# Kernel tuning notes

Measured on AMD Instinct MI355X. Metric: run time of the kernel, lower is better.

Reference implementation:

```python
import jax, jax.numpy as jnp
import numpy as np

N, E, IN, HID, HEADS, ED, OUT = 50000, 600000, 128, 64, 4, 16, 2
NEG_SLOPE = 0.2  # PyG GATv2Conv default negative_slope


def glorot(key, shape):
    fan_in, fan_out = shape[0], shape[-1]
    s = jnp.sqrt(6.0 / (fan_in + fan_out))
    return jax.random.uniform(key, shape, jnp.float32, -s, s)


def setup_inputs() -> dict:
    key = jax.random.key(0)
    ks = jax.random.split(key, 16)
    return {
        "x": jax.random.normal(ks[0], (N, IN), jnp.float32),
        "edge_index": jax.random.randint(ks[1], (2, E), 0, N, jnp.int32),
        "edge_attr": jax.random.normal(ks[2], (E, ED), jnp.float32),
        # conv1: GATv2Conv(IN -> HID, heads=HEADS, concat=True, edge_dim=ED)
        "W1l": glorot(ks[3], (IN, HEADS * HID)), "b1l": jnp.zeros((HEADS * HID,), jnp.float32),
        "W1r": glorot(ks[4], (IN, HEADS * HID)), "b1r": jnp.zeros((HEADS * HID,), jnp.float32),
        "W1e": glorot(ks[5], (ED, HEADS * HID)), "b1e": jnp.zeros((HEADS * HID,), jnp.float32),
        "att1": glorot(ks[6], (HEADS, HID)),
        "bias1": jnp.zeros((HEADS * HID,), jnp.float32),
        # conv2: GATv2Conv(HEADS*HID -> HID, heads=1, concat=False, edge_dim=ED)
        "W2l": glorot(ks[7], (HEADS * HID, HID)), "b2l": jnp.zeros((HID,), jnp.float32),
        "W2r": glorot(ks[8], (HEADS * HID, HID)), "b2r": jnp.zeros((HID,), jnp.float32),
        "W2e": glorot(ks[9], (ED, HID)), "b2e": jnp.zeros((HID,), jnp.float32),
        "att2": glorot(ks[10], (1, HID)),
        "bias2": jnp.zeros((HID,), jnp.float32),
        # edge MLP: Linear(2*HID+ED -> HID) -> ReLU -> Linear(HID -> OUT)
        "Wm1": glorot(ks[11], (2 * HID + ED, HID)), "bm1": jnp.zeros((HID,), jnp.float32),
        "Wm2": glorot(ks[12], (HID, OUT)), "bm2": jnp.zeros((OUT,), jnp.float32),
    }


def gatv2_layer(x, src, dst, edge_attr, Wl, bl, Wr, br, We, be, att, bias, heads, ch, concat):
    n = x.shape[0]
    xl = (x @ Wl + bl).reshape(n, heads, ch)          # lin_l(source)
    xr = (x @ Wr + br).reshape(n, heads, ch)          # lin_r(target)
    xe = (edge_attr @ We + be).reshape(-1, heads, ch)  # lin_edge(edge_attr)
    m = jax.nn.leaky_relu(xl[src] + xr[dst] + xe, NEG_SLOPE)   # [E, H, C]
    logits = jnp.einsum('ehc,hc->eh', m, att)                  # [E, H]
    # segment softmax over incoming edges of each target node
    amax = jax.lax.stop_gradient(jax.ops.segment_max(logits, dst, num_segments=n))
    ex = jnp.exp(logits - amax[dst])
    denom = jax.ops.segment_sum(ex, dst, num_segments=n)
    alpha = ex / denom[dst]                                    # [E, H]
    out = jax.ops.segment_sum(xl[src] * alpha[..., None], dst, num_segments=n)  # [N, H, C]
    out = out.reshape(n, heads * ch) if concat else out.mean(axis=1)
    return out + bias


def reference(x, edge_index, edge_attr, W1l, b1l, W1r, b1r, W1e, b1e, att1, bias1,
              W2l, b2l, W2r, b2r, W2e, b2e, att2, bias2, Wm1, bm1, Wm2, bm2):
    src, dst = edge_index[0], edge_index[1]
    h = jax.nn.relu(gatv2_layer(x, src, dst, edge_attr, W1l, b1l, W1r, b1r, W1e, b1e, att1, bias1, HEADS, HID, True))
    h = jax.nn.relu(gatv2_layer(h, src, dst, edge_attr, W2l, b2l, W2r, b2r, W2e, b2e, att2, bias2, 1, HID, False))
    ef = jnp.concatenate([h[src], h[dst], edge_attr], axis=1)  # [E, 2*HID+ED]
    return jax.nn.relu(ef @ Wm1 + bm1) @ Wm2 + bm2             # [E, OUT]
```

## Files before the change

kernel.cpp:

```cpp
#include <hip/hip_runtime.h>
#include <math.h>

#define NN 50000
#define EE 600000
#define IND 128
#define HIDD 64
#define NH 4
#define EDD 16
#define OUTD 2
#define C1 256

typedef _Float16 h2 __attribute__((ext_vector_type(2)));

__device__ __forceinline__ unsigned short f2bf(float f){
    unsigned b = __float_as_uint(f);
    b += 0x7FFF + ((b >> 16) & 1);
    return (unsigned short)(b >> 16);
}
__device__ __forceinline__ float bf2f(unsigned short h){
    return __uint_as_float(((unsigned)h) << 16);
}
__device__ __forceinline__ h2 f2h2(float a, float b){
    h2 r; r[0] = (_Float16)a; r[1] = (_Float16)b; return r;
}

#if defined(__has_builtin)
#if __has_builtin(__builtin_amdgcn_fdot2)
#define HAS_FDOT2 1
#endif
#if __has_builtin(__builtin_amdgcn_exp2f)
#define HAS_EXP2 1
#endif
#endif
__device__ __forceinline__ float fdot2(h2 a, h2 b, float c){
#ifdef HAS_FDOT2
    return __builtin_amdgcn_fdot2(a, b, c, false);
#else
    return fmaf((float)a[1], (float)b[1], fmaf((float)a[0], (float)b[0], c));
#endif
}
__device__ __forceinline__ float fexp2(float x){
#ifdef HAS_EXP2
    return __builtin_amdgcn_exp2f(x);
#else
    return __expf(x * 0.69314718056f);
#endif
}

__global__ __launch_bounds__(256) void k_hist(const int* __restrict__ dst, int* __restrict__ cnt)
{
    int stride = gridDim.x * blockDim.x;
    for (int e = blockIdx.x * blockDim.x + threadIdx.x; e < EE; e += stride)
        atomicAdd(&cnt[dst[e]], 1);
}

__global__ __launch_bounds__(1024) void k_scan(const int* __restrict__ cnt, int* __restrict__ rs)
{
    __shared__ int wsum[16];
    __shared__ int wpref[16];
    int t = threadIdx.x, lane = t & 63, w = t >> 6;
    int running = 0;
    for (int base = 0; base < NN; base += 1024) {
        int idx = base + t;
        int v = (idx < NN) ? cnt[idx] : 0;
        int sc = v;
#pragma unroll
        for (int off = 1; off < 64; off <<= 1) {
            int u = __shfl_up(sc, off, 64);
            if (lane >= off) sc += u;
        }
        if (lane == 63) wsum[w] = sc;
        __syncthreads();
        if (w == 0 && lane < 16) {
            int x = wsum[lane];
#pragma unroll
            for (int off = 1; off < 16; off <<= 1) {
                int u = __shfl_up(x, off, 64);
                if (lane >= off) x += u;
            }
            wpref[lane] = x;
        }
        __syncthreads();
        int woff = (w == 0) ? 0 : wpref[w - 1];
        if (idx < NN) rs[idx] = running + woff + sc - v;
        running += wpref[15];
        __syncthreads();
    }
    if (t == 0) rs[NN] = running;
}

__global__ __launch_bounds__(256) void k_scatter(
    const int* __restrict__ src, const int* __restrict__ dst,
    const float* __restrict__ ea,
    const int* __restrict__ rs, int* __restrict__ cur,
    int* __restrict__ esrc, _Float16* __restrict__ ea_s, _Float16* __restrict__ ea_h)
{
    int stride = gridDim.x * blockDim.x;
    for (int e = blockIdx.x * blockDim.x + threadIdx.x; e < EE; e += stride) {
        int d = dst[e];
        int p = rs[d] + atomicAdd(&cur[d], 1);
        esrc[p] = src[e];
        const float4* s4 = (const float4*)(ea + (size_t)e * EDD);
        float4 a0 = s4[0], a1 = s4[1], a2 = s4[2], a3 = s4[3];
        union { h2 h[8]; uint4 u[2]; } pk;
        pk.h[0] = f2h2(a0.x, a0.y); pk.h[1] = f2h2(a0.z, a0.w);
        pk.h[2] = f2h2(a1.x, a1.y); pk.h[3] = f2h2(a1.z, a1.w);
        pk.h[4] = f2h2(a2.x, a2.y); pk.h[5] = f2h2(a2.z, a2.w);
        pk.h[6] = f2h2(a3.x, a3.y); pk.h[7] = f2h2(a3.z, a3.w);
        uint4* dq = (uint4*)(ea_s + (size_t)p * EDD);
        dq[0] = pk.u[0]; dq[1] = pk.u[1];
        uint4* hq = (uint4*)(ea_h + (size_t)e * EDD);
        hq[0] = pk.u[0]; hq[1] = pk.u[1];
    }
}

__global__ __launch_bounds__(256) void k_lin1(
    const float* __restrict__ x, const float* __restrict__ Wl, const float* __restrict__ bl,
    const float* __restrict__ Wr, const float* __restrict__ br,
    unsigned short* __restrict__ xl, float* __restrict__ xr)
{
    __shared__ h2 As[32 * 64];
    int t = threadIdx.x;
    int row0 = blockIdx.x * 32;
#pragma unroll
    for (int j = 0; j < 4; ++j) {
        int idx = t + j * 256;
        int r = idx >> 5, c4 = (idx & 31) * 4;
        float4 v = (row0 + r < NN) ? *((const float4*)(x + (size_t)(row0 + r) * IND + c4))
                                   : make_float4(0.f, 0.f, 0.f, 0.f);
        union { h2 h[2]; uint2 u; } pk;
        pk.h[0] = f2h2(v.x, v.y); pk.h[1] = f2h2(v.z, v.w);
        *((uint2*)&As[r * 64 + (c4 >> 1)]) = pk.u;
    }
    __syncthreads();
    float accl[32], accr[32];
    float bL = bl[t], bR = br[t];
#pragma unroll
    for (int i = 0; i < 32; ++i) { accl[i] = bL; accr[i] = bR; }
    for (int k = 0; k < IND; k += 4) {
        h2 wl01 = f2h2(Wl[(k+0) * C1 + t], Wl[(k+1) * C1 + t]);
        h2 wl23 = f2h2(Wl[(k+2) * C1 + t], Wl[(k+3) * C1 + t]);
        h2 wr01 = f2h2(Wr[(k+0) * C1 + t], Wr[(k+1) * C1 + t]);
        h2 wr23 = f2h2(Wr[(k+2) * C1 + t], Wr[(k+3) * C1 + t]);
#pragma unroll
        for (int i = 0; i < 32; ++i) {
            union { uint2 u; h2 h[2]; } av;
            av.u = *((const uint2*)&As[i * 64 + (k >> 1)]);
            accl[i] = fdot2(av.h[0], wl01, accl[i]);
            accl[i] = fdot2(av.h[1], wl23, accl[i]);
            accr[i] = fdot2(av.h[0], wr01, accr[i]);
            accr[i] = fdot2(av.h[1], wr23, accr[i]);
        }
    }
#pragma unroll
    for (int i = 0; i < 32; ++i) {
        int r = row0 + i;
        if (r < NN) {
            xl[(size_t)r * C1 + t] = f2bf(accl[i]);
            xr[(size_t)r * C1 + t] = accr[i];
        }
    }
}

#define GAT1_E(XU, U0, U1) {                                                   \
    float4 xl4 = make_float4(bf2f((XU).x), bf2f((XU).y), bf2f((XU).z), bf2f((XU).w)); \
    union { uint4 u[2]; h2 h[8]; } eu_; eu_.u[0] = (U0); eu_.u[1] = (U1);      \
    float zx = xrb4.x, zy = xrb4.y, zz = xrb4.z, zw = xrb4.w;                  \
    _Pragma("unroll")                                                          \
    for (int kk = 0; kk < 8; ++kk) {                                           \
        h2 ev2 = eu_.h[kk];                                                    \
        zx = fdot2(ev2, Wh[0][kk], zx);                                        \
        zy = fdot2(ev2, Wh[1][kk], zy);                                        \
        zz = fdot2(ev2, Wh[2][kk], zz);                                        \
        zw = fdot2(ev2, Wh[3][kk], zw);                                        \
    }                                                                          \
    zx += xl4.x; zy += xl4.y; zz += xl4.z; zw += xl4.w;                        \
    float vx = fmaxf(zx, 0.2f * zx);                                           \
    float vy = fmaxf(zy, 0.2f * zy);                                           \
    float vz = fmaxf(zz, 0.2f * zz);                                           \
    float vw = fmaxf(zw, 0.2f * zw);                                           \
    float p = vx * sa4.x + vy * sa4.y + vz * sa4.z + vw * sa4.w;               \
    p += __shfl_xor(p, 1, 64);                                                 \
    p += __shfl_xor(p, 2, 64);                                                 \
    p += __shfl_xor(p, 4, 64);                                                 \
    p += __shfl_xor(p, 8, 64);                                                 \
    float el = fexp2(p);                                                       \
    den += el;                                                                 \
    acc.x = fmaf(el, xl4.x, acc.x);                                            \
    acc.y = fmaf(el, xl4.y, acc.y);                                            \
    acc.z = fmaf(el, xl4.z, acc.z);                                            \
    acc.w = fmaf(el, xl4.w, acc.w);                                            \
}

__global__ __launch_bounds__(256) void k_gat1(
    const int* __restrict__ rs, const int* __restrict__ esrc,
    const _Float16* __restrict__ ea_s, const float* __restrict__ We, const float* __restrict__ be,
    const float* __restrict__ att, const unsigned short* __restrict__ xl,
    const float* __restrict__ xr, float* __restrict__ h1)
{
    int t = threadIdx.x, lane = t & 63, w = t >> 6;
    int c4 = lane * 4;
    h2 Wh[4][8];
#pragma unroll
    for (int k = 0; k < 16; ++k) {
        float4 wv = *((const float4*)(We + k * C1 + c4));
        Wh[0][k>>1][k&1] = (_Float16)wv.x;
        Wh[1][k>>1][k&1] = (_Float16)wv.y;
        Wh[2][k>>1][k&1] = (_Float16)wv.z;
        Wh[3][k>>1][k&1] = (_Float16)wv.w;
    }
    float4 sb4 = *((const float4*)(be + c4));
    float4 sa4 = *((const float4*)(att + c4));
    sa4.x *= 1.44269504f; sa4.y *= 1.44269504f;
    sa4.z *= 1.44269504f; sa4.w *= 1.44269504f;
    for (int n = blockIdx.x * 4 + w; n < NN; n += gridDim.x * 4) {
        int beg = __builtin_amdgcn_readfirstlane(rs[n]);
        int end = __builtin_amdgcn_readfirstlane(rs[n + 1]);
        float4 xr4 = *((const float4*)(xr + (size_t)n * C1 + c4));
        float4 xrb4 = make_float4(sb4.x + xr4.x, sb4.y + xr4.y,
                                  sb4.z + xr4.z, sb4.w + xr4.w);
        float den = 0.f;
        float4 acc = make_float4(0.f, 0.f, 0.f, 0.f);
        int i = beg;
        for (; i + 4 <= end; i += 4) {
            int s0 = esrc[i], s1 = esrc[i + 1], s2 = esrc[i + 2], s3 = esrc[i + 3];
            ushort4 xu0 = *((const ushort4*)(xl + (size_t)s0 * C1 + c4));
            ushort4 xu1 = *((const ushort4*)(xl + (size_t)s1 * C1 + c4));
            ushort4 xu2 = *((const ushort4*)(xl + (size_t)s2 * C1 + c4));
            ushort4 xu3 = *((const ushort4*)(xl + (size_t)s3 * C1 + c4));
            const uint4* ep = (const uint4*)(ea_s + (size_t)i * EDD);
            uint4 u0 = ep[0], u1 = ep[1], u2 = ep[2], u3 = ep[3];
            uint4 u4 = ep[4], u5 = ep[5], u6 = ep[6], u7 = ep[7];
            GAT1_E(xu0, u0, u1);
            GAT1_E(xu1, u2, u3);
            GAT1_E(xu2, u4, u5);
            GAT1_E(xu3, u6, u7);
        }
        for (; i < end; ++i) {
            int s0 = esrc[i];
            ushort4 xu0 = *((const ushort4*)(xl + (size_t)s0 * C1 + c4));
            const uint4* ep = (const uint4*)(ea_s + (size_t)i * EDD);
            uint4 u00 = ep[0], u01 = ep[1];
            GAT1_E(xu0, u00, u01);
        }
        float r = den > 0.f ? 1.f / den : 0.f;
        float4 o = make_float4(acc.x * r, acc.y * r, acc.z * r, acc.w * r);
        *((float4*)(h1 + (size_t)n * C1 + c4)) = o;
    }
}

__global__ __launch_bounds__(256) void k_lin2(
    const float* __restrict__ h1acc, const float* __restrict__ bias1,
    const float* __restrict__ Wl, const float* __restrict__ bl,
    const float* __restrict__ Wr, const float* __restrict__ br,
    unsigned short* __restrict__ xl2, float* __restrict__ xr2)
{
    __shared__ h2 As[32 * 130];
    int t = threadIdx.x;
    int row0 = blockIdx.x * 32;
    float b1v = bias1[t];
#pragma unroll
    for (int j = 0; j < 32; ++j) {
        float v = (row0 + j < NN) ? h1acc[(size_t)(row0 + j) * C1 + t] : 0.f;
        v = v + b1v;
        v = v > 0.f ? v : 0.f;
        As[j * 130 + (t >> 1)][t & 1] = (_Float16)v;
    }
    __syncthreads();
    int col = t & 63, g = t >> 6;
    float accl[8], accr[8];
    float bL = bl[col], bR = br[col];
#pragma unroll
    for (int i = 0; i < 8; ++i) { accl[i] = bL; accr[i] = bR; }
    for (int k = 0; k < C1; k += 4) {
        h2 wl01 = f2h2(Wl[(k+0) * HIDD + col], Wl[(k+1) * HIDD + col]);
        h2 wl23 = f2h2(Wl[(k+2) * HIDD + col], Wl[(k+3) * HIDD + col]);
        h2 wr01 = f2h2(Wr[(k+0) * HIDD + col], Wr[(k+1) * HIDD + col]);
        h2 wr23 = f2h2(Wr[(k+2) * HIDD + col], Wr[(k+3) * HIDD + col]);
#pragma unroll
        for (int i = 0; i < 8; ++i) {
            union { uint2 u; h2 h[2]; } av;
            av.u = *((const uint2*)&As[(g * 8 + i) * 130 + (k >> 1)]);
            accl[i] = fdot2(av.h[0], wl01, accl[i]);
            accl[i] = fdot2(av.h[1], wl23, accl[i]);
            accr[i] = fdot2(av.h[0], wr01, accr[i]);
            accr[i] = fdot2(av.h[1], wr23, accr[i]);
        }
    }
#pragma unroll
    for (int i = 0; i < 8; ++i) {
        int r = row0 + g * 8 + i;
        if (r < NN) {
            xl2[(size_t)r * HIDD + col] = f2bf(accl[i]);
            xr2[(size_t)r * HIDD + col] = accr[i];
        }
    }
}

#define GAT2_E(XU, U0, U1) {                                                   \
    float xlv = bf2f(XU);                                                      \
    union { uint4 u[2]; h2 h[8]; } eu_; eu_.u[0] = (U0); eu_.u[1] = (U1);      \
    float z = xrb;                                                             \
    _Pragma("unroll")                                                          \
    for (int kk = 0; kk < 8; ++kk) z = fdot2(eu_.h[kk], Wh2[kk], z);           \
    z += xlv;                                                                  \
    float v = fmaxf(z, 0.2f * z);                                              \
    float p = v * sav;                                                         \
    p += __shfl_xor(p, 1, 64);                                                 \
    p += __shfl_xor(p, 2, 64);                                                 \
    p += __shfl_xor(p, 4, 64);                                                 \
    p += __shfl_xor(p, 8, 64);                                                 \
    p += __shfl_xor(p, 16, 64);                                                \
    p += __shfl_xor(p, 32, 64);                                                \
    float el = fexp2(p);                                                       \
    den += el;                                                                 \
    acc = fmaf(el, xlv, acc);                                                  \
}

__global__ __launch_bounds__(256) void k_gat2(
    const int* __restrict__ rs, const int* __restrict__ esrc,
    const _Float16* __restrict__ ea_s, const float* __restrict__ We, const float* __restrict__ be,
    const float* __restrict__ att, const unsigned short* __restrict__ xl,
    const float* __restrict__ xr, const float* __restrict__ bias2, float* __restrict__ h2v)
{
    int t = threadIdx.x, lane = t & 63, w = t >> 6;
    h2 Wh2[8];
#pragma unroll
    for (int k = 0; k < 16; ++k) Wh2[k>>1][k&1] = (_Float16)We[k * HIDD + lane];
    float bev = be[lane], sav = att[lane] * 1.44269504f, b2 = bias2[lane];
    for (int n = blockIdx.x * 4 + w; n < NN; n += gridDim.x * 4) {
        int beg = __builtin_amdgcn_readfirstlane(rs[n]);
        int end = __builtin_amdgcn_readfirstlane(rs[n + 1]);
        float xrv = xr[(size_t)n * HIDD + lane];
        float xrb = bev + xrv;
        float den = 0.f, acc = 0.f;
        int i = beg;
        for (; i + 4 <= end; i += 4) {
            int s0 = esrc[i], s1 = esrc[i + 1], s2 = esrc[i + 2], s3 = esrc[i + 3];
            unsigned short xu0 = xl[(size_t)s0 * HIDD + lane];
            unsigned short xu1 = xl[(size_t)s1 * HIDD + lane];
            unsigned short xu2 = xl[(size_t)s2 * HIDD + lane];
            unsigned short xu3 = xl[(size_t)s3 * HIDD + lane];
            const uint4* ep = (const uint4*)(ea_s + (size_t)i * EDD);
            uint4 u0 = ep[0], u1 = ep[1], u2 = ep[2], u3 = ep[3];
            uint4 u4 = ep[4], u5 = ep[5], u6 = ep[6], u7 = ep[7];
            GAT2_E(xu0, u0, u1);
            GAT2_E(xu1, u2, u3);
            GAT2_E(xu2, u4, u5);
            GAT2_E(xu3, u6, u7);
        }
        for (; i < end; ++i) {
            int s0 = esrc[i];
            unsigned short xu0 = xl[(size_t)s0 * HIDD + lane];
            const uint4* ep = (const uint4*)(ea_s + (size_t)i * EDD);
            uint4 u00 = ep[0], u01 = ep[1];
            GAT2_E(xu0, u00, u01);
        }
        float r = den > 0.f ? 1.f / den : 0.f;
        float o = fmaf(acc, r, b2);
        h2v[(size_t)n * HIDD + lane] = o > 0.f ? o : 0.f;
    }
}

__global__ __launch_bounds__(256) void k_pq(
    const float* __restrict__ h2, const float* __restrict__ Wm1,
    unsigned short* __restrict__ P, unsigned short* __restrict__ Q)
{
    __shared__ float As[16 * 68];
    int t = threadIdx.x;
    int row0 = blockIdx.x * 16;
    {
        int r = t >> 4, cc = (t & 15) * 4;
        float4 v = *((const float4*)(h2 + (size_t)(row0 + r) * HIDD + cc));
        *((float4*)&As[r * 68 + cc]) = v;
    }
    __syncthreads();
    int col = t & 63, g = t >> 6;
    float accP[4] = {0.f, 0.f, 0.f, 0.f}, accQ[4] = {0.f, 0.f, 0.f, 0.f};
    for (int k = 0; k < 64; k += 4) {
        float wp0 = Wm1[(k+0) * HIDD + col], wp1 = Wm1[(k+1) * HIDD + col];
        float wp2 = Wm1[(k+2) * HIDD + col], wp3 = Wm1[(k+3) * HIDD + col];
        float wq0 = Wm1[(64+k+0) * HIDD + col], wq1 = Wm1[(64+k+1) * HIDD + col];
        float wq2 = Wm1[(64+k+2) * HIDD + col], wq3 = Wm1[(64+k+3) * HIDD + col];
#pragma unroll
        for (int i = 0; i < 4; ++i) {
            float4 a = *((const float4*)&As[(g * 4 + i) * 68 + k]);
            accP[i] = fmaf(a.x, wp0, accP[i]); accP[i] = fmaf(a.y, wp1, accP[i]);
            accP[i] = fmaf(a.z, wp2, accP[i]); accP[i] = fmaf(a.w, wp3, accP[i]);
            accQ[i] = fmaf(a.x, wq0, accQ[i]); accQ[i] = fmaf(a.y, wq1, accQ[i]);
            accQ[i] = fmaf(a.z, wq2, accQ[i]); accQ[i] = fmaf(a.w, wq3, accQ[i]);
        }
    }
#pragma unroll
    for (int i = 0; i < 4; ++i) {
        int r = row0 + g * 4 + i;
        P[(size_t)r * HIDD + col] = f2bf(accP[i]);
        Q[(size_t)r * HIDD + col] = f2bf(accQ[i]);
    }
}

__global__ __launch_bounds__(256) void k_edge(
    const int* __restrict__ src, const int* __restrict__ dst,
    const unsigned short* __restrict__ P, const unsigned short* __restrict__ Q,
    const _Float16* __restrict__ ea_h,
    const float* __restrict__ Wm1, const float* __restrict__ bm1,
    const float* __restrict__ Wm2, const float* __restrict__ bm2,
    float* __restrict__ out)
{
    int t = threadIdx.x, lane = t & 63, w = t >> 6;
    int sub = lane & 15, grp = lane >> 4;
    int c4 = sub * 4;
    h2 Wh[4][8];
#pragma unroll
    for (int k = 0; k < 16; ++k) {
        float4 wv = *((const float4*)(Wm1 + (size_t)(128 + k) * HIDD + c4));
        Wh[0][k>>1][k&1] = (_Float16)wv.x;
        Wh[1][k>>1][k&1] = (_Float16)wv.y;
        Wh[2][k>>1][k&1] = (_Float16)wv.z;
        Wh[3][k>>1][k&1] = (_Float16)wv.w;
    }
    float4 b1 = *((const float4*)(bm1 + c4));
    float w200 = Wm2[(c4+0)*2], w201 = Wm2[(c4+0)*2+1];
    float w210 = Wm2[(c4+1)*2], w211 = Wm2[(c4+1)*2+1];
    float w220 = Wm2[(c4+2)*2], w221 = Wm2[(c4+2)*2+1];
    float w230 = Wm2[(c4+3)*2], w231 = Wm2[(c4+3)*2+1];
    float b20 = bm2[0], b21 = bm2[1];
    for (int base = blockIdx.x * 16 + w * 4; base < EE; base += gridDim.x * 16) {
        int e = base + grp;
        int s = src[e], d = dst[e];
        ushort4 pu = *((const ushort4*)(P + (size_t)s * HIDD + c4));
        ushort4 qu = *((const ushort4*)(Q + (size_t)d * HIDD + c4));
        union { uint4 u[2]; h2 h[8]; } eu_;
        const uint4* ep = (const uint4*)(ea_h + (size_t)e * EDD);
        eu_.u[0] = ep[0]; eu_.u[1] = ep[1];
        float4 hsum = b1;
#pragma unroll
        for (int kk = 0; kk < 8; ++kk) {
            h2 ev2 = eu_.h[kk];
            hsum.x = fdot2(ev2, Wh[0][kk], hsum.x);
            hsum.y = fdot2(ev2, Wh[1][kk], hsum.y);
            hsum.z = fdot2(ev2, Wh[2][kk], hsum.z);
            hsum.w = fdot2(ev2, Wh[3][kk], hsum.w);
        }
        float hx = fmaxf(hsum.x + bf2f(pu.x) + bf2f(qu.x), 0.f);
        float hy = fmaxf(hsum.y + bf2f(pu.y) + bf2f(qu.y), 0.f);
        float hz = fmaxf(hsum.z + bf2f(pu.z) + bf2f(qu.z), 0.f);
        float hw = fmaxf(hsum.w + bf2f(pu.w) + bf2f(qu.w), 0.f);
        float p0 = hx * w200 + hy * w210 + hz * w220 + hw * w230;
        float p1 = hx * w201 + hy * w211 + hz * w221 + hw * w231;
        p0 += __shfl_xor(p0, 1, 64);
        p0 += __shfl_xor(p0, 2, 64);
        p0 += __shfl_xor(p0, 4, 64);
        p0 += __shfl_xor(p0, 8, 64);
        p1 += __shfl_xor(p1, 1, 64);
        p1 += __shfl_xor(p1, 2, 64);
        p1 += __shfl_xor(p1, 4, 64);
        p1 += __shfl_xor(p1, 8, 64);
        if (sub == 0) ((float2*)out)[e] = make_float2(p0 + b20, p1 + b21);
    }
}

extern "C" void kernel_launch(void* const* d_in, const int* in_sizes, int n_in,
                              void* d_out, int out_size, void* d_ws, size_t ws_size,
                              hipStream_t stream)
{
    const float* x    = (const float*)d_in[0];
    const int*   ei   = (const int*)d_in[1];
    const float* ea   = (const float*)d_in[2];
    const float* W1l  = (const float*)d_in[3];
    const float* b1l  = (const float*)d_in[4];
    const float* W1r  = (const float*)d_in[5];
    const float* b1r  = (const float*)d_in[6];
    const float* W1e  = (const float*)d_in[7];
    const float* b1e  = (const float*)d_in[8];
    const float* att1 = (const float*)d_in[9];
    const float* bias1= (const float*)d_in[10];
    const float* W2l  = (const float*)d_in[11];
    const float* b2l  = (const float*)d_in[12];
    const float* W2r  = (const float*)d_in[13];
    const float* b2r  = (const float*)d_in[14];
    const float* W2e  = (const float*)d_in[15];
    const float* b2e  = (const float*)d_in[16];
    const float* att2 = (const float*)d_in[17];
    const float* bias2= (const float*)d_in[18];
    const float* Wm1  = (const float*)d_in[19];
    const float* bm1  = (const float*)d_in[20];
    const float* Wm2  = (const float*)d_in[21];
    const float* bm2  = (const float*)d_in[22];
    float* out = (float*)d_out;
    const int* srcp = ei;
    const int* dstp = ei + EE;

    float* ws = (float*)d_ws;
    const size_t NC1  = (size_t)NN * C1;
    const size_t NH64 = (size_t)NN * HIDD;
    const size_t EAH  = (size_t)EE * EDD / 2;
    size_t o_xl1u = 0;
    size_t o_xr1  = o_xl1u + NC1 / 2;
    size_t o_xl2u = 0;
    size_t o_xr2  = o_xl2u + NH64 / 2;
    size_t o_h2   = o_xr2 + NH64;
    size_t o_Pu   = o_h2 + NH64;
    size_t o_Qu   = o_Pu + NH64 / 2;
    size_t o_h1   = o_xr1 + NC1;
    size_t o_ea_s = o_h1 + NC1;
    size_t o_ea_h = o_ea_s + EAH;
    size_t o_cnt  = o_ea_h + EAH;
    size_t o_rs   = o_cnt + 2 * (size_t)NN;
    size_t o_esrc = o_rs + (size_t)NN + 8;

    unsigned short* xl1u = (unsigned short*)(ws + o_xl1u);
    unsigned short* xl2u = (unsigned short*)(ws + o_xl2u);
    unsigned short* Pu   = (unsigned short*)(ws + o_Pu);
    unsigned short* Qu   = (unsigned short*)(ws + o_Qu);
    _Float16* ea_s = (_Float16*)(ws + o_ea_s);
    _Float16* ea_h = (_Float16*)(ws + o_ea_h);
    int* cnt  = (int*)(ws + o_cnt);
    int* cur  = cnt + NN;
    int* rs   = (int*)(ws + o_rs);
    int* esrc = (int*)(ws + o_esrc);

    hipMemsetAsync(cnt, 0, 2 * (size_t)NN * sizeof(int), stream);

    dim3 blk(256);
    k_hist<<<1024, blk, 0, stream>>>(dstp, cnt);
    k_scan<<<1, 1024, 0, stream>>>(cnt, rs);
    k_scatter<<<1024, blk, 0, stream>>>(srcp, dstp, ea, rs, cur, esrc, ea_s, ea_h);

    k_lin1<<<1563, blk, 0, stream>>>(x, W1l, b1l, W1r, b1r, xl1u, ws + o_xr1);
    k_gat1<<<2048, blk, 0, stream>>>(rs, esrc, ea_s, W1e, b1e, att1,
                                     xl1u, ws + o_xr1, ws + o_h1);
    k_lin2<<<1563, blk, 0, stream>>>(ws + o_h1, bias1, W2l, b2l, W2r, b2r,
                                     xl2u, ws + o_xr2);
    k_gat2<<<2048, blk, 0, stream>>>(rs, esrc, ea_s, W2e, b2e, att2,
                                     xl2u, ws + o_xr2, bias2, ws + o_h2);
    k_pq<<<3125, blk, 0, stream>>>(ws + o_h2, Wm1, Pu, Qu);
    k_edge<<<2048, blk, 0, stream>>>(srcp, dstp, Pu, Qu, ea_h,
                                     Wm1, bm1, Wm2, bm2, out);
}
```

Measured before the change: 609.2 us.

## Merge scatter with lin1 launch and process four edges per wave in gat2

Fuses the CSR scatter kernel and the first linear layer into one launch, with the block index choosing the role, so the two independent jobs can run concurrently and one launch is saved. Rewrites the layer-2 attention kernel so each wave splits into four 16-lane groups. Each group handles a different edge and each lane owns four channels, using vectorized loads and a shorter shuffle reduction, with a cross-group reduction at the end. This raises memory-level parallelism on low-degree nodes, at the cost of more registers for the replicated weights and masked work on the tail edges.

Result: faster. 592.7 us (median of 2 runs) (-2.7%).

```diff
diff --git a/kernel.cpp b/kernel.cpp
--- a/kernel.cpp
+++ b/kernel.cpp
@@ -89,39 +89,38 @@
     if (t == 0) rs[NN] = running;
 }
 
-__global__ __launch_bounds__(256) void k_scatter(
+__global__ __launch_bounds__(256) void k_scatter_lin1(
     const int* __restrict__ src, const int* __restrict__ dst,
     const float* __restrict__ ea,
     const int* __restrict__ rs, int* __restrict__ cur,
-    int* __restrict__ esrc, _Float16* __restrict__ ea_s, _Float16* __restrict__ ea_h)
-{
-    int stride = gridDim.x * blockDim.x;
-    for (int e = blockIdx.x * blockDim.x + threadIdx.x; e < EE; e += stride) {
-        int d = dst[e];
-        int p = rs[d] + atomicAdd(&cur[d], 1);
-        esrc[p] = src[e];
-        const float4* s4 = (const float4*)(ea + (size_t)e * EDD);
-        float4 a0 = s4[0], a1 = s4[1], a2 = s4[2], a3 = s4[3];
-        union { h2 h[8]; uint4 u[2]; } pk;
-        pk.h[0] = f2h2(a0.x, a0.y); pk.h[1] = f2h2(a0.z, a0.w);
-        pk.h[2] = f2h2(a1.x, a1.y); pk.h[3] = f2h2(a1.z, a1.w);
-        pk.h[4] = f2h2(a2.x, a2.y); pk.h[5] = f2h2(a2.z, a2.w);
-        pk.h[6] = f2h2(a3.x, a3.y); pk.h[7] = f2h2(a3.z, a3.w);
-        uint4* dq = (uint4*)(ea_s + (size_t)p * EDD);
-        dq[0] = pk.u[0]; dq[1] = pk.u[1];
-        uint4* hq = (uint4*)(ea_h + (size_t)e * EDD);
-        hq[0] = pk.u[0]; hq[1] = pk.u[1];
-    }
-}
-
-__global__ __launch_bounds__(256) void k_lin1(
+    int* __restrict__ esrc, _Float16* __restrict__ ea_s, _Float16* __restrict__ ea_h,
     const float* __restrict__ x, const float* __restrict__ Wl, const float* __restrict__ bl,
     const float* __restrict__ Wr, const float* __restrict__ br,
     unsigned short* __restrict__ xl, float* __restrict__ xr)
 {
     __shared__ h2 As[32 * 64];
+    if (blockIdx.x < 1024) {
+        int stride = 1024 * 256;
+        for (int e = blockIdx.x * 256 + threadIdx.x; e < EE; e += stride) {
+            int d = dst[e];
+            int p = rs[d] + atomicAdd(&cur[d], 1);
+            esrc[p] = src[e];
+            const float4* s4 = (const float4*)(ea + (size_t)e * EDD);
+            float4 a0 = s4[0], a1 = s4[1], a2 = s4[2], a3 = s4[3];
+            union { h2 h[8]; uint4 u[2]; } pk;
+            pk.h[0] = f2h2(a0.x, a0.y); pk.h[1] = f2h2(a0.z, a0.w);
+            pk.h[2] = f2h2(a1.x, a1.y); pk.h[3] = f2h2(a1.z, a1.w);
+            pk.h[4] = f2h2(a2.x, a2.y); pk.h[5] = f2h2(a2.z, a2.w);
+            pk.h[6] = f2h2(a3.x, a3.y); pk.h[7] = f2h2(a3.z, a3.w);
+            uint4* dq = (uint4*)(ea_s + (size_t)p * EDD);
+            dq[0] = pk.u[0]; dq[1] = pk.u[1];
+            uint4* hq = (uint4*)(ea_h + (size_t)e * EDD);
+            hq[0] = pk.u[0]; hq[1] = pk.u[1];
+        }
+        return;
+    }
     int t = threadIdx.x;
-    int row0 = blockIdx.x * 32;
+    int row0 = (blockIdx.x - 1024) * 32;
 #pragma unroll
     for (int j = 0; j < 4; ++j) {
         int idx = t + j * 256;
@@ -297,26 +296,6 @@
     }
 }
 
-#define GAT2_E(XU, U0, U1) {                                                   \
-    float xlv = bf2f(XU);                                                      \
-    union { uint4 u[2]; h2 h[8]; } eu_; eu_.u[0] = (U0); eu_.u[1] = (U1);      \
-    float z = xrb;                                                             \
-    _Pragma("unroll")                                                          \
-    for (int kk = 0; kk < 8; ++kk) z = fdot2(eu_.h[kk], Wh2[kk], z);           \
-    z += xlv;                                                                  \
-    float v = fmaxf(z, 0.2f * z);                                              \
-    float p = v * sav;                                                         \
-    p += __shfl_xor(p, 1, 64);                                                 \
-    p += __shfl_xor(p, 2, 64);                                                 \
-    p += __shfl_xor(p, 4, 64);                                                 \
-    p += __shfl_xor(p, 8, 64);                                                 \
-    p += __shfl_xor(p, 16, 64);                                                \
-    p += __shfl_xor(p, 32, 64);                                                \
-    float el = fexp2(p);                                                       \
-    den += el;                                                                 \
-    acc = fmaf(el, xlv, acc);                                                  \
-}
-
 __global__ __launch_bounds__(256) void k_gat2(
     const int* __restrict__ rs, const int* __restrict__ esrc,
     const _Float16* __restrict__ ea_s, const float* __restrict__ We, const float* __restrict__ be,
@@ -324,41 +303,80 @@
     const float* __restrict__ xr, const float* __restrict__ bias2, float* __restrict__ h2v)
 {
     int t = threadIdx.x, lane = t & 63, w = t >> 6;
-    h2 Wh2[8];
-#pragma unroll
-    for (int k = 0; k < 16; ++k) Wh2[k>>1][k&1] = (_Float16)We[k * HIDD + lane];
-    float bev = be[lane], sav = att[lane] * 1.44269504f, b2 = bias2[lane];
+    int sub = lane & 15, grp = lane >> 4;
+    int c4 = sub * 4;
+    h2 Wh[4][8];
+#pragma unroll
+    for (int k = 0; k < 16; ++k) {
+        float4 wv = *((const float4*)(We + k * HIDD + c4));
+        Wh[0][k>>1][k&1] = (_Float16)wv.x;
+        Wh[1][k>>1][k&1] = (_Float16)wv.y;
+        Wh[2][k>>1][k&1] = (_Float16)wv.z;
+        Wh[3][k>>1][k&1] = (_Float16)wv.w;
+    }
+    float4 be4 = *((const float4*)(be + c4));
+    float4 sa4 = *((const float4*)(att + c4));
+    sa4.x *= 1.44269504f; sa4.y *= 1.44269504f;
+    sa4.z *= 1.44269504f; sa4.w *= 1.44269504f;
+    float4 b24 = *((const float4*)(bias2 + c4));
     for (int n = blockIdx.x * 4 + w; n < NN; n += gridDim.x * 4) {
         int beg = __builtin_amdgcn_readfirstlane(rs[n]);
         int end = __builtin_amdgcn_readfirstlane(rs[n + 1]);
-        float xrv = xr[(size_t)n * HIDD + lane];
-        float xrb = bev + xrv;
-        float den = 0.f, acc = 0.f;
-        int i = beg;
-        for (; i + 4 <= end; i += 4) {
-            int s0 = esrc[i], s1 = esrc[i + 1], s2 = esrc[i + 2], s3 = esrc[i + 3];
-            unsigned short xu0 = xl[(size_t)s0 * HIDD + lane];
-            unsigned short xu1 = xl[(size_t)s1 * HIDD + lane];
-            unsigned short xu2 = xl[(size_t)s2 * HIDD + lane];
-            unsigned short xu3 = xl[(size_t)s3 * HIDD + lane];
-            const uint4* ep = (const uint4*)(ea_s + (size_t)i * EDD);
-            uint4 u0 = ep[0], u1 = ep[1], u2 = ep[2], u3 = ep[3];
-            uint4 u4 = ep[4], u5 = ep[5], u6 = ep[6], u7 = ep[7];
-            GAT2_E(xu0, u0, u1);
-            GAT2_E(xu1, u2, u3);
-            GAT2_E(xu2, u4, u5);
-            GAT2_E(xu3, u6, u7);
-        }
-        for (; i < end; ++i) {
-            int s0 = esrc[i];
-            unsigned short xu0 = xl[(size_t)s0 * HIDD + lane];
-            const uint4* ep = (const uint4*)(ea_s + (size_t)i * EDD);
-            uint4 u00 = ep[0], u01 = ep[1];
-            GAT2_E(xu0, u00, u01);
-        }
+        float4 xr4 = *((const float4*)(xr + (size_t)n * HIDD + c4));
+        float4 xrb4 = make_float4(be4.x + xr4.x, be4.y + xr4.y,
+                                  be4.z + xr4.z, be4.w + xr4.w);
+        float den = 0.f;
+        float4 acc = make_float4(0.f, 0.f, 0.f, 0.f);
+        for (int i = beg; i < end; i += 4) {
+            int e = i + grp;
+            int ec = e < end ? e : end - 1;
+            int s = esrc[ec];
+            ushort4 xu = *((const ushort4*)(xl + (size_t)s * HIDD + c4));
+            const uint4* ep = (const uint4*)(ea_s + (size_t)ec * EDD);
+            union { uint4 u[2]; h2 h[8]; } eu_;
+            eu_.u[0] = ep[0]; eu_.u[1] = ep[1];
+            float4 xl4 = make_float4(bf2f(xu.x), bf2f(xu.y), bf2f(xu.z), bf2f(xu.w));
+            float zx = xrb4.x, zy = xrb4.y, zz = xrb4.z, zw = xrb4.w;
+#pragma unroll
+            for (int kk = 0; kk < 8; ++kk) {
+                h2 ev2 = eu_.h[kk];
+                zx = fdot2(ev2, Wh[0][kk], zx);
+                zy = fdot2(ev2, Wh[1][kk], zy);
+                zz = fdot2(ev2, Wh[2][kk], zz);
+                zw = fdot2(ev2, Wh[3][kk], zw);
+            }
+            zx += xl4.x; zy += xl4.y; zz += xl4.z; zw += xl4.w;
+            float vx = fmaxf(zx, 0.2f * zx);
+            float vy = fmaxf(zy, 0.2f * zy);
+            float vz = fmaxf(zz, 0.2f * zz);
+            float vw = fmaxf(zw, 0.2f * zw);
+            float p = vx * sa4.x + vy * sa4.y + vz * sa4.z + vw * sa4.w;
+            p += __shfl_xor(p, 1, 64);
+            p += __shfl_xor(p, 2, 64);
+            p += __shfl_xor(p, 4, 64);
+            p += __shfl_xor(p, 8, 64);
+            float el = (e < end) ? fexp2(p) : 0.f;
+            den += el;
+            acc.x = fmaf(el, xl4.x, acc.x);
+            acc.y = fmaf(el, xl4.y, acc.y);
+            acc.z = fmaf(el, xl4.z, acc.z);
+            acc.w = fmaf(el, xl4.w, acc.w);
+        }
+        den += __shfl_xor(den, 16, 64);
+        den += __shfl_xor(den, 32, 64);
+        acc.x += __shfl_xor(acc.x, 16, 64); acc.x += __shfl_xor(acc.x, 32, 64);
+        acc.y += __shfl_xor(acc.y, 16, 64); acc.y += __shfl_xor(acc.y, 32, 64);
+        acc.z += __shfl_xor(acc.z, 16, 64); acc.z += __shfl_xor(acc.z, 32, 64);
+        acc.w += __shfl_xor(acc.w, 16, 64); acc.w += __shfl_xor(acc.w, 32, 64);
         float r = den > 0.f ? 1.f / den : 0.f;
-        float o = fmaf(acc, r, b2);
-        h2v[(size_t)n * HIDD + lane] = o > 0.f ? o : 0.f;
+        if (grp == 0) {
+            float4 o;
+            o.x = fmaxf(fmaf(acc.x, r, b24.x), 0.f);
+            o.y = fmaxf(fmaf(acc.y, r, b24.y), 0.f);
+            o.z = fmaxf(fmaf(acc.z, r, b24.z), 0.f);
+            o.w = fmaxf(fmaf(acc.w, r, b24.w), 0.f);
+            *((float4*)(h2v + (size_t)n * HIDD + c4)) = o;
+        }
     }
 }
 
@@ -525,9 +543,10 @@
     dim3 blk(256);
     k_hist<<<1024, blk, 0, stream>>>(dstp, cnt);
     k_scan<<<1, 1024, 0, stream>>>(cnt, rs);
-    k_scatter<<<1024, blk, 0, stream>>>(srcp, dstp, ea, rs, cur, esrc, ea_s, ea_h);
-
-    k_lin1<<<1563, blk, 0, stream>>>(x, W1l, b1l, W1r, b1r, xl1u, ws + o_xr1);
+    k_scatter_lin1<<<2587, blk, 0, stream>>>(srcp, dstp, ea, rs, cur, esrc,
+                                             ea_s, ea_h,
+                                             x, W1l, b1l, W1r, b1r,
+                                             xl1u, ws + o_xr1);
     k_gat1<<<2048, blk, 0, stream>>>(rs, esrc, ea_s, W1e, b1e, att1,
                                      xl1u, ws + o_xr1, ws + o_h1);
     k_lin2<<<1563, blk, 0, stream>>>(ws + o_h1, bias1, W2l, b2l, W2r, b2r,
```
